# Kernel tuning notes

Hardware: AMD Instinct MI355X
Metric: run time of the kernel (lower is better)

## Reference

```python
import jax, jax.numpy as jnp
import numpy as np

M = 100000   # rows of sparse matrix B
K = 100000   # cols of sparse matrix B / rows of dense A
N = 64       # cols of dense A
NNZ = 1600000

def setup_inputs() -> dict:
    key = jax.random.key(0)
    k1, k2, k3, k4 = jax.random.split(key, 4)
    vals = jax.random.normal(k1, (NNZ,), dtype=jnp.float32)
    A = jax.random.normal(k2, (K, N), dtype=jnp.float32)
    rows = jax.random.randint(k3, (NNZ,), 0, M, dtype=jnp.int32)
    cols = jax.random.randint(k4, (NNZ,), 0, K, dtype=jnp.int32)
    return {"vals": vals, "A": A, "rows": rows, "cols": cols}

def reference(vals, A, rows, cols):
    # out[m, n] = sum_{k in nnz(row m)} B[m,k] * A[k,n]
    contrib = A[cols] * vals[:, None]            # [NNZ, N] gather + scale
    out = jax.ops.segment_sum(contrib, rows, num_segments=M)  # scatter-add -> [M, N]
    return out
```

## Files before the change

### kernel.cpp

```cpp
#include <hip/hip_runtime.h>
#include <hip/hip_bf16.h>


#define NCOLS      64
#define RPB        64
#define RPB_SHIFT  6
#define NBLK       256
#define BT         256
#define CAP_S      8192
#define CAP_R      2048
#define SCAP       12
#define MAXNB      1568

__global__ void spmm_scatter_atomic(const float* __restrict__ vals,
                                    const float* __restrict__ A,
                                    const int* __restrict__ rows,
                                    const int* __restrict__ cols,
                                    float* __restrict__ out,
                                    int nnz) {
    int t = blockIdx.x * blockDim.x + threadIdx.x;
    int e = t >> 4;
    int q = t & 15;
    if (e >= nnz) return;
    float v = vals[e];
    int   r = rows[e];
    int   c = cols[e];
    const float4 a = *reinterpret_cast<const float4*>(A + (size_t)c * NCOLS + q * 4);
    float* o = out + (size_t)r * NCOLS + q * 4;
    atomicAdd(o + 0, v * a.x);
    atomicAdd(o + 1, v * a.y);
    atomicAdd(o + 2, v * a.z);
    atomicAdd(o + 3, v * a.w);
}

__global__ void conv_a_bf16(const float* __restrict__ A, uint* __restrict__ Abf,
                            int n) {
    int i = blockIdx.x * blockDim.x + threadIdx.x;
    int idx = i << 3;
    if (idx >= n) return;
    const uint4 u0 = *reinterpret_cast<const uint4*>(A + idx);
    const uint4 u1 = *reinterpret_cast<const uint4*>(A + idx + 4);
    auto bf = [](uint u) -> uint { return (u + 0x7FFFu + ((u >> 16) & 1u)) >> 16; };
    uint4 o;
    o.x = bf(u0.x) | (bf(u0.y) << 16);
    o.y = bf(u0.z) | (bf(u0.w) << 16);
    o.z = bf(u1.x) | (bf(u1.y) << 16);
    o.w = bf(u1.z) | (bf(u1.w) << 16);
    *reinterpret_cast<uint4*>(Abf + (i << 2)) = o;
}

__global__ void __launch_bounds__(BT)
sort_scatter(const float* __restrict__ vals,
             const int* __restrict__ rows,
             const int* __restrict__ cols,
             int2* __restrict__ pvc,
             int* __restrict__ tab,
             int nnz, int chunk, int NB) {
    __shared__ int2 sorted[CAP_S];
    __shared__ int  cnt[MAXNB];
    __shared__ int  sc[BT];

    int j = blockIdx.x, t = threadIdx.x;
    int base = j * chunk;
    int n = nnz - base;
    if (n > chunk) n = chunk;
    if (n < 0) n = 0;
    int nv = n >> 2;

    for (int i = t; i < NB; i += BT) cnt[i] = 0;
    __syncthreads();

    const int4* r4p = reinterpret_cast<const int4*>(rows + base);
    for (int i = t; i < nv; i += BT) {
        int4 r = r4p[i];
        atomicAdd(&cnt[r.x >> RPB_SHIFT], 1);
        atomicAdd(&cnt[r.y >> RPB_SHIFT], 1);
        atomicAdd(&cnt[r.z >> RPB_SHIFT], 1);
        atomicAdd(&cnt[r.w >> RPB_SHIFT], 1);
    }
    for (int i = (nv << 2) + t; i < n; i += BT)
        atomicAdd(&cnt[rows[base + i] >> RPB_SHIFT], 1);
    __syncthreads();

    int spt = (NB + BT - 1) / BT;
    int lo = t * spt, hi = min(lo + spt, NB);
    int s = 0;
    for (int i = lo; i < hi; ++i) s += cnt[i];
    sc[t] = s;
    __syncthreads();
    for (int off = 1; off < BT; off <<= 1) {
        int u = (t >= off) ? sc[t - off] : 0;
        __syncthreads();
        sc[t] += u;
        __syncthreads();
    }
    int run = sc[t] - s;
    for (int i = lo; i < hi; ++i) { int c = cnt[i]; cnt[i] = run; run += c; }
    __syncthreads();

    for (int b = t; b < NB; b += BT) tab[(size_t)j * (NB + 1) + b] = base + cnt[b];
    if (t == 0) tab[(size_t)j * (NB + 1) + NB] = base + n;
    __syncthreads();

    const float4* v4p = reinterpret_cast<const float4*>(vals + base);
    const int4*   c4p = reinterpret_cast<const int4*>(cols + base);
    for (int i = t; i < nv; i += BT) {
        int4 r = r4p[i]; float4 v = v4p[i]; int4 c = c4p[i];
        int slot;
        slot = atomicAdd(&cnt[r.x >> RPB_SHIFT], 1);
        sorted[slot] = make_int2(__float_as_int(v.x), c.x | ((r.x & (RPB - 1)) << 17));
        slot = atomicAdd(&cnt[r.y >> RPB_SHIFT], 1);
        sorted[slot] = make_int2(__float_as_int(v.y), c.y | ((r.y & (RPB - 1)) << 17));
        slot = atomicAdd(&cnt[r.z >> RPB_SHIFT], 1);
        sorted[slot] = make_int2(__float_as_int(v.z), c.z | ((r.z & (RPB - 1)) << 17));
        slot = atomicAdd(&cnt[r.w >> RPB_SHIFT], 1);
        sorted[slot] = make_int2(__float_as_int(v.w), c.w | ((r.w & (RPB - 1)) << 17));
    }
    for (int i = (nv << 2) + t; i < n; i += BT) {
        int e = base + i;
        int r = rows[e];
        int slot = atomicAdd(&cnt[r >> RPB_SHIFT], 1);
        sorted[slot] = make_int2(__float_as_int(vals[e]),
                                 cols[e] | ((r & (RPB - 1)) << 17));
    }
    __syncthreads();

    int4* pvc4 = reinterpret_cast<int4*>(pvc + base);
    int nh = n >> 1;
    for (int i = t; i < nh; i += BT) {
        int2 a = sorted[2 * i], b2 = sorted[2 * i + 1];
        pvc4[i] = make_int4(a.x, a.y, b2.x, b2.y);
    }
    if ((n & 1) && t == 0) pvc[base + n - 1] = sorted[n - 1];
}

template<int USEBF>
__global__ void __launch_bounds__(BT)
spmm_reduce_rs(const int2* __restrict__ pvc,
               const int* __restrict__ tab,
               const float* __restrict__ A,
               const uint* __restrict__ Abf,
               float* __restrict__ out,
               int M, int NB) {
    __shared__ int2 sorted[CAP_R];
    __shared__ int  cnt[RPB];
    __shared__ int  off[RPB + 1];

    int b = blockIdx.x, t = threadIdx.x;
    int sS = tab[(size_t)t * (NB + 1) + b];
    int sE = tab[(size_t)t * (NB + 1) + b + 1];
    int len = sE - sS;

    if (t < RPB) cnt[t] = 0;
    __syncthreads();

    int2 st[SCAP];
    #pragma unroll
    for (int i = 0; i < SCAP; ++i) {
        if (i < len) {
            st[i] = pvc[sS + i];
            atomicAdd(&cnt[(st[i].y >> 17) & (RPB - 1)], 1);
        }
    }
    for (int i = SCAP; i < len; ++i)
        atomicAdd(&cnt[(pvc[sS + i].y >> 17) & (RPB - 1)], 1);
    __syncthreads();

    if (t < RPB) {
        int v = cnt[t];
        int s = v;
        #pragma unroll
        for (int d = 1; d < RPB; d <<= 1) {
            int u = __shfl_up(s, d, 64);
            if (t >= d) s += u;
        }
        off[t + 1] = s;
        if (t == 0) off[0] = 0;
        cnt[t] = s - v;
    }
    __syncthreads();

    int total = off[RPB];
    int row0 = b << RPB_SHIFT;
    int nrow = min(RPB, M - row0);

    if (total > CAP_R) {
        for (int i = t; i < nrow * NCOLS; i += BT) out[(size_t)row0 * NCOLS + i] = 0.f;
        __syncthreads();
        for (int e = sS; e < sE; ++e) {
            int2 vc = pvc[e];
            float v = __int_as_float(vc.x);
            int   c = vc.y & 0x1FFFF;
            int   rl = (vc.y >> 17) & (RPB - 1);
            for (int nn = 0; nn < NCOLS; ++nn)
                atomicAdd(&out[(size_t)(row0 + rl) * NCOLS + nn],
                          v * A[(size_t)c * NCOLS + nn]);
        }
        return;
    }

    #pragma unroll
    for (int i = 0; i < SCAP; ++i) {
        if (i < len) {
            int slot = atomicAdd(&cnt[(st[i].y >> 17) & (RPB - 1)], 1);
            sorted[slot] = st[i];
        }
    }
    for (int i = SCAP; i < len; ++i) {
        int2 vc = pvc[sS + i];
        int slot = atomicAdd(&cnt[(vc.y >> 17) & (RPB - 1)], 1);
        sorted[slot] = vc;
    }
    __syncthreads();

    int lane = t & 3;
    int grp  = t >> 2;
    float acc[16];
    #pragma unroll
    for (int i = 0; i < 16; ++i) acc[i] = 0.f;

    int s0 = off[grp], s1 = off[grp + 1];

    if (USEBF) {
        auto fma16 = [&](uint4 u0, uint4 u1, float v) {
            acc[0]  += v * __uint_as_float(u0.x << 16);
            acc[1]  += v * __uint_as_float(u0.x & 0xFFFF0000u);
            acc[2]  += v * __uint_as_float(u0.y << 16);
            acc[3]  += v * __uint_as_float(u0.y & 0xFFFF0000u);
            acc[4]  += v * __uint_as_float(u0.z << 16);
            acc[5]  += v * __uint_as_float(u0.z & 0xFFFF0000u);
            acc[6]  += v * __uint_as_float(u0.w << 16);
            acc[7]  += v * __uint_as_float(u0.w & 0xFFFF0000u);
            acc[8]  += v * __uint_as_float(u1.x << 16);
            acc[9]  += v * __uint_as_float(u1.x & 0xFFFF0000u);
            acc[10] += v * __uint_as_float(u1.y << 16);
            acc[11] += v * __uint_as_float(u1.y & 0xFFFF0000u);
            acc[12] += v * __uint_as_float(u1.z << 16);
            acc[13] += v * __uint_as_float(u1.z & 0xFFFF0000u);
            acc[14] += v * __uint_as_float(u1.w << 16);
            acc[15] += v * __uint_as_float(u1.w & 0xFFFF0000u);
        };
        int e = s0;
        for (; e + 4 <= s1; e += 4) {
            int2 vc0 = sorted[e], vc1 = sorted[e + 1];
            int2 vc2 = sorted[e + 2], vc3 = sorted[e + 3];
            const uint4* p0 = reinterpret_cast<const uint4*>(
                Abf + ((size_t)(vc0.y & 0x1FFFF) << 5) + (lane << 3));
            const uint4* p1 = reinterpret_cast<const uint4*>(
                Abf + ((size_t)(vc1.y & 0x1FFFF) << 5) + (lane << 3));
            const uint4* p2 = reinterpret_cast<const uint4*>(
                Abf + ((size_t)(vc2.y & 0x1FFFF) << 5) + (lane << 3));
            const uint4* p3 = reinterpret_cast<const uint4*>(
                Abf + ((size_t)(vc3.y & 0x1FFFF) << 5) + (lane << 3));
            uint4 a0 = p0[0], b0 = p0[1];
            uint4 a1 = p1[0], b1 = p1[1];
            uint4 a2 = p2[0], b2 = p2[1];
            uint4 a3 = p3[0], b3 = p3[1];
            fma16(a0, b0, __int_as_float(vc0.x));
            fma16(a1, b1, __int_as_float(vc1.x));
            fma16(a2, b2, __int_as_float(vc2.x));
            fma16(a3, b3, __int_as_float(vc3.x));
        }
        for (; e < s1; ++e) {
            int2 vc = sorted[e];
            const uint4* p = reinterpret_cast<const uint4*>(
                Abf + ((size_t)(vc.y & 0x1FFFF) << 5) + (lane << 3));
            uint4 u0 = p[0], u1 = p[1];
            fma16(u0, u1, __int_as_float(vc.x));
        }
    } else {
        auto fma16f = [&](float4 a0, float4 a1, float4 a2, float4 a3, float v) {
            acc[0]  += v * a0.x; acc[1]  += v * a0.y;
            acc[2]  += v * a0.z; acc[3]  += v * a0.w;
            acc[4]  += v * a1.x; acc[5]  += v * a1.y;
            acc[6]  += v * a1.z; acc[7]  += v * a1.w;
            acc[8]  += v * a2.x; acc[9]  += v * a2.y;
            acc[10] += v * a2.z; acc[11] += v * a2.w;
            acc[12] += v * a3.x; acc[13] += v * a3.y;
            acc[14] += v * a3.z; acc[15] += v * a3.w;
        };
        int e = s0;
        for (; e + 2 <= s1; e += 2) {
            int2 vc0 = sorted[e], vc1 = sorted[e + 1];
            const float4* p0 = reinterpret_cast<const float4*>(
                A + ((size_t)(vc0.y & 0x1FFFF) << 6) + (lane << 4));
            const float4* p1 = reinterpret_cast<const float4*>(
                A + ((size_t)(vc1.y & 0x1FFFF) << 6) + (lane << 4));
            float4 x0 = p0[0], x1 = p0[1], x2 = p0[2], x3 = p0[3];
            float4 y0 = p1[0], y1 = p1[1], y2 = p1[2], y3 = p1[3];
            fma16f(x0, x1, x2, x3, __int_as_float(vc0.x));
            fma16f(y0, y1, y2, y3, __int_as_float(vc1.x));
        }
        for (; e < s1; ++e) {
            int2 vc = sorted[e];
            const float4* p = reinterpret_cast<const float4*>(
                A + ((size_t)(vc.y & 0x1FFFF) << 6) + (lane << 4));
            float4 x0 = p[0], x1 = p[1], x2 = p[2], x3 = p[3];
            fma16f(x0, x1, x2, x3, __int_as_float(vc.x));
        }
    }

    int m = row0 + grp;
    if (m < M) {
        float4* o = reinterpret_cast<float4*>(out + (size_t)m * NCOLS + (lane << 4));
        o[0] = make_float4(acc[0],  acc[1],  acc[2],  acc[3]);
        o[1] = make_float4(acc[4],  acc[5],  acc[6],  acc[7]);
        o[2] = make_float4(acc[8],  acc[9],  acc[10], acc[11]);
        o[3] = make_float4(acc[12], acc[13], acc[14], acc[15]);
    }
}

extern "C" void kernel_launch(void* const* d_in, const int* in_sizes, int n_in,
                              void* d_out, int out_size, void* d_ws, size_t ws_size,
                              hipStream_t stream) {
    const float* vals = (const float*)d_in[0];
    const float* A    = (const float*)d_in[1];
    const int*   rows = (const int*)d_in[2];
    const int*   cols = (const int*)d_in[3];
    float*       out  = (float*)d_out;

    const int nnz = in_sizes[0];
    const int na  = in_sizes[1];
    const int M   = out_size / NCOLS;
    const int K   = na / NCOLS;

    const int NB    = (M + RPB - 1) >> RPB_SHIFT;
    const int chunk = (((nnz + NBLK - 1) / NBLK) + 3) & ~3;

    size_t off_tab = 0;
    size_t tab_sz  = (size_t)NBLK * (NB + 1) * 4;
    size_t off_pvc = (off_tab + tab_sz + 15) & ~(size_t)15;
    size_t off_abf = (off_pvc + (size_t)nnz * 8 + 15) & ~(size_t)15;
    size_t need_f32 = off_pvc + (size_t)nnz * 8;
    size_t need_bf  = off_abf + (size_t)na * 2;

    if (need_f32 > ws_size || chunk > CAP_S || NB > MAXNB ||
        K > (1 << 17) || (na & 7) != 0) {
        hipMemsetAsync(d_out, 0, (size_t)out_size * sizeof(float), stream);
        int threads_total = nnz * 16;
        int block = 256;
        int grid = (threads_total + block - 1) / block;
        spmm_scatter_atomic<<<grid, block, 0, stream>>>(vals, A, rows, cols, out, nnz);
        return;
    }

    char* ws = (char*)d_ws;
    int*  tab = (int*)(ws + off_tab);
    int2* pvc = (int2*)(ws + off_pvc);
    uint* abf = (uint*)(ws + off_abf);

    const bool use_bf = (need_bf <= ws_size);

    if (use_bf) {
        int nthr = na / 8;
        conv_a_bf16<<<(nthr + 255) / 256, 256, 0, stream>>>(A, abf, na);
    }
    sort_scatter<<<NBLK, BT, 0, stream>>>(vals, rows, cols, pvc, tab, nnz, chunk, NB);
    if (use_bf)
        spmm_reduce_rs<1><<<NB, BT, 0, stream>>>(pvc, tab, A, abf, out, M, NB);
    else
        spmm_reduce_rs<0><<<NB, BT, 0, stream>>>(pvc, tab, A, abf, out, M, NB);
}
```

Measured before the change: 80.68 us.

## Fuse bf16 conversion of A into the sort kernel and widen blocks to 1024

Removes the separate conv_a_bf16 launch by having each sort block first convert a slice of A to bf16, then do its bucket sort. The sort kernel's block size grows from 256 to 1024 threads, so counting, prefix scan and scatter run with more parallelism per chunk. This saves one kernel launch and lets conversion traffic share the sort's blocks. The cost is a longer 1024-wide scan with more barriers, and only 256 large blocks, which may limit occupancy.

```diff
diff --git a/kernel.cpp b/kernel.cpp
--- a/kernel.cpp
+++ b/kernel.cpp
@@ -7,6 +7,7 @@
 #define RPB_SHIFT  6
 #define NBLK       256
 #define BT         256
+#define BT_S       1024
 #define CAP_S      8192
 #define CAP_R      2048
 #define SCAP       12
@@ -33,62 +34,66 @@
     atomicAdd(o + 3, v * a.w);
 }
 
-__global__ void conv_a_bf16(const float* __restrict__ A, uint* __restrict__ Abf,
-                            int n) {
-    int i = blockIdx.x * blockDim.x + threadIdx.x;
-    int idx = i << 3;
-    if (idx >= n) return;
-    const uint4 u0 = *reinterpret_cast<const uint4*>(A + idx);
-    const uint4 u1 = *reinterpret_cast<const uint4*>(A + idx + 4);
-    auto bf = [](uint u) -> uint { return (u + 0x7FFFu + ((u >> 16) & 1u)) >> 16; };
-    uint4 o;
-    o.x = bf(u0.x) | (bf(u0.y) << 16);
-    o.y = bf(u0.z) | (bf(u0.w) << 16);
-    o.z = bf(u1.x) | (bf(u1.y) << 16);
-    o.w = bf(u1.z) | (bf(u1.w) << 16);
-    *reinterpret_cast<uint4*>(Abf + (i << 2)) = o;
-}
-
-__global__ void __launch_bounds__(BT)
-sort_scatter(const float* __restrict__ vals,
-             const int* __restrict__ rows,
-             const int* __restrict__ cols,
-             int2* __restrict__ pvc,
-             int* __restrict__ tab,
-             int nnz, int chunk, int NB) {
+__global__ void __launch_bounds__(BT_S)
+sort_conv(const float* __restrict__ vals,
+          const int* __restrict__ rows,
+          const int* __restrict__ cols,
+          const float* __restrict__ A,
+          uint* __restrict__ Abf,
+          int2* __restrict__ pvc,
+          int* __restrict__ tab,
+          int nnz, int chunk, int NB, int na8, int doconv) {
     __shared__ int2 sorted[CAP_S];
     __shared__ int  cnt[MAXNB];
-    __shared__ int  sc[BT];
+    __shared__ int  sc[BT_S];
 
     int j = blockIdx.x, t = threadIdx.x;
+
+    if (doconv) {
+        int e8pb = (na8 + gridDim.x - 1) / gridDim.x;
+        int clo = j * e8pb, chi = min(clo + e8pb, na8);
+        auto bf = [](uint u) -> uint { return (u + 0x7FFFu + ((u >> 16) & 1u)) >> 16; };
+        for (int i = clo + t; i < chi; i += BT_S) {
+            int idx = i << 3;
+            const uint4 u0 = *reinterpret_cast<const uint4*>(A + idx);
+            const uint4 u1 = *reinterpret_cast<const uint4*>(A + idx + 4);
+            uint4 o;
+            o.x = bf(u0.x) | (bf(u0.y) << 16);
+            o.y = bf(u0.z) | (bf(u0.w) << 16);
+            o.z = bf(u1.x) | (bf(u1.y) << 16);
+            o.w = bf(u1.z) | (bf(u1.w) << 16);
+            *reinterpret_cast<uint4*>(Abf + (i << 2)) = o;
+        }
+    }
+
     int base = j * chunk;
     int n = nnz - base;
     if (n > chunk) n = chunk;
     if (n < 0) n = 0;
     int nv = n >> 2;
 
-    for (int i = t; i < NB; i += BT) cnt[i] = 0;
+    for (int i = t; i < NB; i += BT_S) cnt[i] = 0;
     __syncthreads();
 
     const int4* r4p = reinterpret_cast<const int4*>(rows + base);
-    for (int i = t; i < nv; i += BT) {
+    for (int i = t; i < nv; i += BT_S) {
         int4 r = r4p[i];
         atomicAdd(&cnt[r.x >> RPB_SHIFT], 1);
         atomicAdd(&cnt[r.y >> RPB_SHIFT], 1);
         atomicAdd(&cnt[r.z >> RPB_SHIFT], 1);
         atomicAdd(&cnt[r.w >> RPB_SHIFT], 1);
     }
-    for (int i = (nv << 2) + t; i < n; i += BT)
+    for (int i = (nv << 2) + t; i < n; i += BT_S)
         atomicAdd(&cnt[rows[base + i] >> RPB_SHIFT], 1);
     __syncthreads();
 
-    int spt = (NB + BT - 1) / BT;
+    int spt = (NB + BT_S - 1) / BT_S;
     int lo = t * spt, hi = min(lo + spt, NB);
     int s = 0;
     for (int i = lo; i < hi; ++i) s += cnt[i];
     sc[t] = s;
     __syncthreads();
-    for (int off = 1; off < BT; off <<= 1) {
+    for (int off = 1; off < BT_S; off <<= 1) {
         int u = (t >= off) ? sc[t - off] : 0;
         __syncthreads();
         sc[t] += u;
@@ -98,13 +103,13 @@
     for (int i = lo; i < hi; ++i) { int c = cnt[i]; cnt[i] = run; run += c; }
     __syncthreads();
 
-    for (int b = t; b < NB; b += BT) tab[(size_t)j * (NB + 1) + b] = base + cnt[b];
+    for (int b = t; b < NB; b += BT_S) tab[(size_t)j * (NB + 1) + b] = base + cnt[b];
     if (t == 0) tab[(size_t)j * (NB + 1) + NB] = base + n;
     __syncthreads();
 
     const float4* v4p = reinterpret_cast<const float4*>(vals + base);
     const int4*   c4p = reinterpret_cast<const int4*>(cols + base);
-    for (int i = t; i < nv; i += BT) {
+    for (int i = t; i < nv; i += BT_S) {
         int4 r = r4p[i]; float4 v = v4p[i]; int4 c = c4p[i];
         int slot;
         slot = atomicAdd(&cnt[r.x >> RPB_SHIFT], 1);
@@ -116,7 +121,7 @@
         slot = atomicAdd(&cnt[r.w >> RPB_SHIFT], 1);
         sorted[slot] = make_int2(__float_as_int(v.w), c.w | ((r.w & (RPB - 1)) << 17));
     }
-    for (int i = (nv << 2) + t; i < n; i += BT) {
+    for (int i = (nv << 2) + t; i < n; i += BT_S) {
         int e = base + i;
         int r = rows[e];
         int slot = atomicAdd(&cnt[r >> RPB_SHIFT], 1);
@@ -127,7 +132,7 @@
 
     int4* pvc4 = reinterpret_cast<int4*>(pvc + base);
     int nh = n >> 1;
-    for (int i = t; i < nh; i += BT) {
+    for (int i = t; i < nh; i += BT_S) {
         int2 a = sorted[2 * i], b2 = sorted[2 * i + 1];
         pvc4[i] = make_int4(a.x, a.y, b2.x, b2.y);
     }
@@ -350,12 +355,10 @@
     uint* abf = (uint*)(ws + off_abf);
 
     const bool use_bf = (need_bf <= ws_size);
-
-    if (use_bf) {
-        int nthr = na / 8;
-        conv_a_bf16<<<(nthr + 255) / 256, 256, 0, stream>>>(A, abf, na);
-    }
-    sort_scatter<<<NBLK, BT, 0, stream>>>(vals, rows, cols, pvc, tab, nnz, chunk, NB);
+    const int  na8    = na >> 3;
+
+    sort_conv<<<NBLK, BT_S, 0, stream>>>(vals, rows, cols, A, abf, pvc, tab,
+                                         nnz, chunk, NB, na8, use_bf ? 1 : 0);
     if (use_bf)
         spmm_reduce_rs<1><<<NB, BT, 0, stream>>>(pvc, tab, A, abf, out, M, NB);
     else
```

Measured after the change: 76.41 us (median of 2 runs). 1.06x faster.
